# Performance work log

Measured on AMD Instinct MI355X. Metric: run time of the kernel, lower is better.

Reference implementation:

```python
import jax, jax.numpy as jnp
import numpy as np

B, T, C, H = 8, 1024, 1024, 16  # batch, seq, n_embd, n_head


def setup_inputs() -> dict:
    key = jax.random.key(0)
    ks = jax.random.split(key, 5)
    scale = 1.0 / np.sqrt(C)
    return {
        "x": jax.random.normal(ks[0], (B, T, C), dtype=jnp.float32),
        "Wqkv": jax.random.normal(ks[1], (C, 3 * C), dtype=jnp.float32) * scale,
        "bqkv": jax.random.normal(ks[2], (3 * C,), dtype=jnp.float32) * 0.02,
        "Wproj": jax.random.normal(ks[3], (C, C), dtype=jnp.float32) * scale,
        "bproj": jax.random.normal(ks[4], (C,), dtype=jnp.float32) * 0.02,
        "n_head": H,
    }


def reference(x, Wqkv, bqkv, Wproj, bproj, n_head):
    Bb, Tt, Cc = x.shape
    hd = Cc // n_head  # head dim
    qkv = x @ Wqkv + bqkv                      # [B,T,3C]
    q, k, v = jnp.split(qkv, 3, axis=-1)       # each [B,T,C]
    # [B,T,C] -> [B,H,T,hd]
    def to_heads(t):
        return t.reshape(Bb, Tt, n_head, hd).transpose(0, 2, 1, 3)
    q, k, v = to_heads(q), to_heads(k), to_heads(v)
    scores = jnp.einsum("bhqd,bhkd->bhqk", q, k) / jnp.sqrt(jnp.asarray(hd, q.dtype))
    causal = jnp.tril(jnp.ones((Tt, Tt), dtype=bool))
    scores = jnp.where(causal, scores, jnp.asarray(-jnp.inf, scores.dtype))
    attn = jax.nn.softmax(scores, axis=-1)
    y = jnp.einsum("bhqk,bhkd->bhqd", attn, v)  # [B,H,T,hd]
    y = y.transpose(0, 2, 1, 3).reshape(Bb, Tt, Cc)
    return y @ Wproj + bproj
```

## Files before the change

kernel.cpp:

```cpp
#include <hip/hip_runtime.h>
#include <hip/hip_bf16.h>
#include <math.h>
#include <type_traits>

#define Bz 8
#define Tz 1024
#define Cz 1024
#define Hz 16
#define HDz 64
#define Mz (Bz*Tz)
#define N1 (3*Cz)
#define QKN 2048

typedef __attribute__((ext_vector_type(8))) short short8;
typedef __attribute__((ext_vector_type(4))) short short4v;
typedef __attribute__((ext_vector_type(4))) float floatx4;

template<int V> using IC = std::integral_constant<int, V>;

__device__ __forceinline__ unsigned short f2bf(float f) {
    unsigned u = __float_as_uint(f);
    return (unsigned short)((u + 0x7FFFu + ((u >> 16) & 1u)) >> 16);
}

__device__ __forceinline__ unsigned pkbf(float a, float b) {
    __hip_bfloat162 h = __float22bfloat162_rn(make_float2(a, b));
    return *(unsigned*)&h;
}

__device__ __forceinline__ void gload16(const void* g, void* l) {
    __builtin_amdgcn_global_load_lds(
        (const __attribute__((address_space(1))) unsigned int*)g,
        (__attribute__((address_space(3))) unsigned int*)l, 16, 0, 0);
}

__global__ __launch_bounds__(256) void prep_kernel(
    const float* __restrict__ x, unsigned short* __restrict__ xb,
    const float* __restrict__ Wqkv, unsigned short* __restrict__ Wqkvt,
    const float* __restrict__ Wproj, unsigned short* __restrict__ Wprojt)
{
    __shared__ float tile[32][33];
    const int bid = blockIdx.x;
    const int tid = threadIdx.x;
    if (bid < 8192) {
        int i = bid * 256 + tid;
        float4 v = *(const float4*)&x[(size_t)i * 4];
        ushort4 o;
        o.x = f2bf(v.x); o.y = f2bf(v.y); o.z = f2bf(v.z); o.w = f2bf(v.w);
        *(ushort4*)&xb[(size_t)i * 4] = o;
        return;
    }
    const float* W; unsigned short* Wt; int K, N, n0, k0;
    if (bid < 11264) {
        int b = bid - 8192;  W = Wqkv;  Wt = Wqkvt;  K = Cz; N = N1;
        n0 = (b % 96) * 32;  k0 = (b / 96) * 32;
    } else {
        int b = bid - 11264; W = Wproj; Wt = Wprojt; K = Cz; N = Cz;
        n0 = (b % 32) * 32;  k0 = (b / 32) * 32;
    }
    const int tx = tid & 31, ty = tid >> 5;
#pragma unroll
    for (int i = 0; i < 4; ++i)
        tile[ty + i * 8][tx] = W[(size_t)(k0 + ty + i * 8) * N + n0 + tx];
    __syncthreads();
#pragma unroll
    for (int i = 0; i < 4; ++i)
        Wt[(size_t)(n0 + ty + i * 8) * K + k0 + tx] = f2bf(tile[tx][ty + i * 8]);
}

template<int NI, int MODE, int NXB>
__global__ __launch_bounds__(512) void gemm8p(
    const unsigned short* __restrict__ A,
    const unsigned short* __restrict__ Bt,
    const float* __restrict__ bias,
    void* __restrict__ Cout, unsigned short* __restrict__ VtG)
{
    constexpr int LDSB = 16384 + NI * 4096;
    constexpr int NT = 16;
    constexpr int NBLK = (Mz / 256) * NXB;
    constexpr int CHUNK = NBLK / 8;
    constexpr int NOUT = NXB * NI * 64;
    __shared__ unsigned short lds[2 * LDSB];

    const int tid = threadIdx.x;
    const int lane = tid & 63;
    const int w = tid >> 6;
    const int wm = w >> 2, wn = w & 3;
    const int quad = lane >> 4, m16 = lane & 15;
    const int sw7 = m16 & 7;

    int wg = blockIdx.x;
    wg = (wg & 7) * CHUNK + (wg >> 3);
    const int bx = wg % NXB, by = wg / NXB;
    const int row0 = by * 256, col0 = bx * (NI * 64);

    const int srow = tid >> 3;
    const int scol = ((tid & 7) ^ (srow & 7)) * 8;
    const unsigned short* sA[2][2];
    const unsigned short* sBu[NI];
#pragma unroll
    for (int h = 0; h < 2; ++h)
#pragma unroll
        for (int c = 0; c < 2; ++c)
            sA[h][c] = A + (size_t)(row0 + h * 128 + c * 64 + srow) * Cz + scol;
#pragma unroll
    for (int u = 0; u < NI; ++u)
        sBu[u] = Bt + (size_t)(col0 + u * 64 + srow) * Cz + scol;

    auto stage_tile = [&](int kt, int db) {
        unsigned short* base = &lds[db * LDSB];
#pragma unroll
        for (int u = 0; u < NI; ++u)
            gload16(sBu[u] + kt * 64, base + 16384 + u * 4096 + w * 512);
        gload16(sA[0][0] + kt * 64, base + w * 512);
        gload16(sA[0][1] + kt * 64, base + w * 512 + 4096);
        gload16(sA[1][0] + kt * 64, base + 8192 + w * 512);
        gload16(sA[1][1] + kt * 64, base + 8192 + w * 512 + 4096);
    };

    float bv[NI];
#pragma unroll
    for (int ni = 0; ni < NI; ++ni)
        bv[ni] = bias[col0 + wn * (NI * 16) + ni * 16 + m16];

    floatx4 acc[8][NI];
#pragma unroll
    for (int mi = 0; mi < 8; ++mi)
#pragma unroll
        for (int ni = 0; ni < NI; ++ni)
            acc[mi][ni] = (floatx4){0.f, 0.f, 0.f, 0.f};

    stage_tile(0, 0);
    stage_tile(1, 1);

    int b = 0;
#pragma unroll 1
    for (int kt = 0; kt < NT; ++kt, b ^= 1) {
        if (kt < NT - 1) {
            if constexpr (NI == 3) asm volatile("s_waitcnt vmcnt(7)" ::: "memory");
            else                   asm volatile("s_waitcnt vmcnt(6)" ::: "memory");
        } else {
            asm volatile("s_waitcnt vmcnt(0)" ::: "memory");
        }
        asm volatile("s_barrier" ::: "memory");

        const unsigned short* lA = &lds[b * LDSB];
        const unsigned short* lB = &lds[b * LDSB + 16384];

        auto loadA = [&](auto pc, short8 (&af)[2][2]) {
            constexpr int p = decltype(pc)::value;
            constexpr int hf = p >> 1;
#pragma unroll
            for (int j = 0; j < 2; ++j) {
                const int ra = ((p & 1) * 64 + j * 32 + wm * 16 + m16) * 64;
#pragma unroll
                for (int ks = 0; ks < 2; ++ks)
                    af[j][ks] = *(const short8*)&lA[hf * 8192 + ra + ((((ks << 2) | quad) ^ sw7) << 3)];
            }
        };

        short8 bfr[NI][2];
#pragma unroll
        for (int ni = 0; ni < NI; ++ni) {
            const int rb = (wn * (NI * 16) + ni * 16 + m16) * 64;
#pragma unroll
            for (int ks = 0; ks < 2; ++ks)
                bfr[ni][ks] = *(const short8*)&lB[rb + ((((ks << 2) | quad) ^ sw7) << 3)];
        }

        auto cluster = [&](auto pc, short8 (&af)[2][2]) {
            constexpr int p = decltype(pc)::value;
            __builtin_amdgcn_s_setprio(1);
#pragma unroll
            for (int ks = 0; ks < 2; ++ks)
#pragma unroll
                for (int j = 0; j < 2; ++j)
#pragma unroll
                    for (int ni = 0; ni < NI; ++ni)
                        acc[p * 2 + j][ni] = __builtin_amdgcn_mfma_f32_16x16x32_bf16(
                            af[j][ks], bfr[ni][ks], acc[p * 2 + j][ni], 0, 0, 0);
            __builtin_amdgcn_s_setprio(0);
        };

        short8 afA[2][2], afB[2][2];
        loadA(IC<0>{}, afA);
        __builtin_amdgcn_sched_barrier(0);
        loadA(IC<1>{}, afB);
        __builtin_amdgcn_sched_barrier(0);
        asm volatile("s_waitcnt lgkmcnt(4)" ::: "memory");
        __builtin_amdgcn_sched_barrier(0);
        cluster(IC<0>{}, afA);
        loadA(IC<2>{}, afA);
        __builtin_amdgcn_sched_barrier(0);
        asm volatile("s_waitcnt lgkmcnt(4)" ::: "memory");
        __builtin_amdgcn_sched_barrier(0);
        cluster(IC<1>{}, afB);
        loadA(IC<3>{}, afB);
        __builtin_amdgcn_sched_barrier(0);
        asm volatile("s_waitcnt lgkmcnt(4)" ::: "memory");
        __builtin_amdgcn_sched_barrier(0);
        cluster(IC<2>{}, afA);
        asm volatile("s_waitcnt lgkmcnt(0)" ::: "memory");
        __builtin_amdgcn_sched_barrier(0);
        if (kt + 2 < NT) {
            asm volatile("s_barrier" ::: "memory");
            stage_tile(kt + 2, b);
        }
        __builtin_amdgcn_sched_barrier(0);
        cluster(IC<3>{}, afB);
    }

    if constexpr (MODE == 0) {
#pragma unroll
        for (int ni = 0; ni < NI; ++ni) {
            const int c = col0 + wn * (NI * 16) + ni * 16 + m16;
#pragma unroll
            for (int mi = 0; mi < 8; ++mi)
#pragma unroll
                for (int reg = 0; reg < 4; ++reg) {
                    const int r = row0 + mi * 32 + wm * 16 + quad * 4 + reg;
                    ((float*)Cout)[(size_t)r * NOUT + c] = acc[mi][ni][reg] + bv[ni];
                }
        }
    } else {
#pragma unroll
        for (int ni = 0; ni < NI; ++ni) {
            const int c0 = col0 + wn * (NI * 16) + ni * 16;
            if (c0 < 2048) {
#pragma unroll
                for (int mi = 0; mi < 8; ++mi)
#pragma unroll
                    for (int reg = 0; reg < 4; ++reg) {
                        const int r = row0 + mi * 32 + wm * 16 + quad * 4 + reg;
                        ((unsigned short*)Cout)[(size_t)r * QKN + c0 + m16] =
                            f2bf(acc[mi][ni][reg] + bv[ni]);
                    }
            } else {
                const int cb = c0 - 2048;
                const int hsel = cb >> 6;
                const int dd = (cb & 63) + m16;
                const int bq = row0 >> 10;
                const int tb = row0 & 1023;
                unsigned short* drow = VtG
                    + (size_t)(bq * Hz + hsel) * (HDz * Tz)
                    + (size_t)dd * Tz + tb;
#pragma unroll
                for (int mi = 0; mi < 8; ++mi) {
                    const int t = mi * 32 + wm * 16 + quad * 4;
                    unsigned pk[2];
                    pk[0] = pkbf(acc[mi][ni][0] + bv[ni], acc[mi][ni][1] + bv[ni]);
                    pk[1] = pkbf(acc[mi][ni][2] + bv[ni], acc[mi][ni][3] + bv[ni]);
                    *(uint2*)&drow[t] = *(uint2*)pk;
                }
            }
        }
    }
}

__global__ __launch_bounds__(128) void attn_kernel(const unsigned short* __restrict__ qkb,
    const unsigned short* __restrict__ VtG, unsigned short* __restrict__ attb)
{
    __shared__ unsigned short Ks[2][64 * 64];
    __shared__ unsigned short Vs[2][64 * 64];

    const int bx = blockIdx.x;
    const int bh = blockIdx.y;
    const int b = bh >> 4, h = bh & 15;
    const int tid = threadIdx.x, lane = tid & 63, w = tid >> 6;
    const int quad = lane >> 4, m16 = lane & 15;
    const int qis[2] = {15 - bx, bx};

    const unsigned short* Kb = qkb + (size_t)(b * Tz) * QKN + Cz + h * HDz;
    const unsigned short* Vb = VtG + (size_t)bh * (HDz * Tz);

    const int l3 = lane >> 3, l7 = lane & 7;
    const int gsw = ((l7 ^ l3) << 3);
    const int sw = m16 & 7;
    const int p0 = (quad ^ sw) << 3;

    short8 onesf = (short8){0,0,0,0,0,0,0,0};
    if (m16 == 0) {
        const short one = (short)0x3F80;
        onesf = (short8){one,one,one,one,one,one,one,one};
    }

    int srow[4];
#pragma unroll
    for (int i = 0; i < 4; ++i) srow[i] = w * 32 + i * 8 + l3;

#pragma unroll
    for (int i = 0; i < 4; ++i) {
        gload16(Kb + (size_t)srow[i] * QKN + gsw, &Ks[0][(w * 4 + i) * 512]);
        gload16(Vb + (size_t)srow[i] * Tz + gsw, &Vs[0][(w * 4 + i) * 512]);
    }

    int buf = 0;
    for (int t = 0; t < 2; ++t) {
        const int qi = qis[t];

        short8 qf[2][2];
        int qrow[2];
#pragma unroll
        for (int mi = 0; mi < 2; ++mi) {
            qrow[mi] = qi * 64 + w * 32 + mi * 16 + m16;
            const size_t rq = (size_t)(b * Tz + qrow[mi]) * QKN + h * HDz;
            qf[mi][0] = *(const short8*)&qkb[rq + quad * 8];
            qf[mi][1] = *(const short8*)&qkb[rq + 32 + quad * 8];
        }

        floatx4 of[2][4];
#pragma unroll
        for (int mi = 0; mi < 2; ++mi)
#pragma unroll
            for (int dc = 0; dc < 4; ++dc) of[mi][dc] = (floatx4){0.f, 0.f, 0.f, 0.f};
        floatx4 lsum[2];
        lsum[0] = (floatx4){0.f, 0.f, 0.f, 0.f};
        lsum[1] = (floatx4){0.f, 0.f, 0.f, 0.f};

        auto tile_body = [&](auto diag_c) {
            constexpr bool DIAG = decltype(diag_c)::value;
            short8 pf[2][2];
#pragma unroll
            for (int m0 = 0; m0 < 4; ++m0) {
                if (DIAG && w == 0 && m0 >= 2) continue;
                const unsigned short* kr = &Ks[buf][(m0 * 16 + m16) * 64];
                short8 kf0 = *(const short8*)&kr[p0];
                short8 kf1 = *(const short8*)&kr[p0 ^ 32];
#pragma unroll
                for (int mi = 0; mi < 2; ++mi) {
                    floatx4 st = (floatx4){0.f, 0.f, 0.f, 0.f};
                    st = __builtin_amdgcn_mfma_f32_16x16x32_bf16(kf0, qf[mi][0], st, 0, 0, 0);
                    st = __builtin_amdgcn_mfma_f32_16x16x32_bf16(kf1, qf[mi][1], st, 0, 0, 0);
                    float p[4];
#pragma unroll
                    for (int reg = 0; reg < 4; ++reg) {
                        p[reg] = exp2f(st[reg] * 0.18033688f);
                        if (DIAG) {
                            int key = m0 * 16 + quad * 4 + reg;
                            int qr  = w * 32 + mi * 16 + m16;
                            p[reg] = (key <= qr) ? p[reg] : 0.f;
                        }
                    }
                    unsigned* pp = (unsigned*)&pf[mi][m0 >> 1];
                    pp[(m0 & 1) * 2 + 0] = pkbf(p[0], p[1]);
                    pp[(m0 & 1) * 2 + 1] = pkbf(p[2], p[3]);
                }
            }
#pragma unroll
            for (int kg = 0; kg < 2; ++kg) {
                if (DIAG && w == 0 && kg == 1) continue;
#pragma unroll
                for (int mi = 0; mi < 2; ++mi)
                    lsum[mi] = __builtin_amdgcn_mfma_f32_16x16x32_bf16(onesf, pf[mi][kg], lsum[mi], 0, 0, 0);
#pragma unroll
                for (int dc = 0; dc < 4; ++dc) {
                    const unsigned short* vrow = &Vs[buf][(dc * 16 + m16) * 64];
                    const int g0 = kg * 4 + (quad >> 1);
                    const int off = (quad & 1) * 4;
                    short4v v0 = *(const short4v*)&vrow[((g0 ^ sw) << 3) + off];
                    short4v v1 = *(const short4v*)&vrow[(((g0 + 2) ^ sw) << 3) + off];
                    short8 vf;
                    vf[0] = v0[0]; vf[1] = v0[1]; vf[2] = v0[2]; vf[3] = v0[3];
                    vf[4] = v1[0]; vf[5] = v1[1]; vf[6] = v1[2]; vf[7] = v1[3];
#pragma unroll
                    for (int mi = 0; mi < 2; ++mi)
                        of[mi][dc] = __builtin_amdgcn_mfma_f32_16x16x32_bf16(vf, pf[mi][kg], of[mi][dc], 0, 0, 0);
                }
            }
        };

        for (int ki = 0; ki <= qi; ++ki) {
            __syncthreads();
            const int nk = (ki < qi) ? (ki + 1) : (t == 0 ? 0 : -1);
            if (nk >= 0) {
                const size_t ko = (size_t)nk * 64;
#pragma unroll
                for (int i = 0; i < 4; ++i) {
                    gload16(Kb + (ko + srow[i]) * QKN + gsw, &Ks[buf ^ 1][(w * 4 + i) * 512]);
                    gload16(Vb + (size_t)srow[i] * Tz + ko + gsw, &Vs[buf ^ 1][(w * 4 + i) * 512]);
                }
            }
            if (ki == qi) tile_body(std::true_type{});
            else          tile_body(std::false_type{});
            buf ^= 1;
        }

#pragma unroll
        for (int mi = 0; mi < 2; ++mi) {
            const float l = __shfl(lsum[mi][0], m16);
            const float inv = 1.f / l;
            const size_t orow = (size_t)(b * Tz + qrow[mi]) * Cz + h * HDz;
#pragma unroll
            for (int dc = 0; dc < 4; ++dc) {
                ushort4 o;
                o.x = f2bf(of[mi][dc][0] * inv);
                o.y = f2bf(of[mi][dc][1] * inv);
                o.z = f2bf(of[mi][dc][2] * inv);
                o.w = f2bf(of[mi][dc][3] * inv);
                *(ushort4*)&attb[orow + dc * 16 + quad * 4] = o;
            }
        }
    }
}

extern "C" void kernel_launch(void* const* d_in, const int* in_sizes, int n_in,
                              void* d_out, int out_size, void* d_ws, size_t ws_size,
                              hipStream_t stream)
{
    const float* x     = (const float*)d_in[0];
    const float* Wqkv  = (const float*)d_in[1];
    const float* bqkv  = (const float*)d_in[2];
    const float* Wproj = (const float*)d_in[3];
    const float* bproj = (const float*)d_in[4];
    float* out = (float*)d_out;

    unsigned short* xb     = (unsigned short*)d_ws;
    unsigned short* Wqkvt  = xb + (size_t)Mz * Cz;
    unsigned short* Wprojt = Wqkvt + (size_t)N1 * Cz;
    unsigned short* qkb    = Wprojt + (size_t)Cz * Cz;
    unsigned short* VtG    = qkb + (size_t)Mz * QKN;
    unsigned short* attb   = xb;

    prep_kernel<<<12288, 256, 0, stream>>>(x, xb, Wqkv, Wqkvt, Wproj, Wprojt);

    gemm8p<3, 2, 16><<<512, 512, 0, stream>>>(xb, Wqkvt, bqkv, qkb, VtG);

    attn_kernel<<<dim3(8, Bz * Hz), 128, 0, stream>>>(qkb, VtG, attb);

    gemm8p<2, 0, 8><<<256, 512, 0, stream>>>(attb, Wprojt, bproj, out, nullptr);
}
```

Before: 236.0 us.

## Replace QKV GEMM with 128x192-tile kernel using split A/B staging

Adds a dedicated QKV projection kernel that uses 128x192 output tiles and 1024 workgroups, replacing the previous 256-row tile kernel launched with 512 workgroups. The new kernel staggers the A and B global loads across two half-iterations, raises MFMA priority during compute, and remaps block IDs for locality. The smaller LDS footprint and launch_bounds(512,4) aim to raise occupancy and smooth the memory pipeline, at the cost of less data reuse per tile. It also adds an explicit vmcnt(0) wait after the bias loads so they do not disturb the vmcnt-based pipeline accounting.

```diff
diff --git a/kernel.cpp b/kernel.cpp
--- a/kernel.cpp
+++ b/kernel.cpp
@@ -68,6 +68,158 @@
         Wt[(size_t)(n0 + ty + i * 8) * K + k0 + tx] = f2bf(tile[tx][ty + i * 8]);
 }
 
+__global__ __launch_bounds__(512, 4) void gemm128_qkv(
+    const unsigned short* __restrict__ A,
+    const unsigned short* __restrict__ Bt,
+    const float* __restrict__ bias,
+    unsigned short* __restrict__ Cqk, unsigned short* __restrict__ VtG)
+{
+    __shared__ unsigned short lds[2 * 20480];
+    constexpr int NT = 16;
+
+    const int tid = threadIdx.x;
+    const int lane = tid & 63;
+    const int w = tid >> 6;
+    const int wm = w >> 2, wn = w & 3;
+    const int quad = lane >> 4, m16 = lane & 15;
+    const int sw7 = m16 & 7;
+
+    int wg = blockIdx.x;
+    wg = (wg & 7) * 128 + (wg >> 3);
+    const int bx = wg & 15, by = wg >> 4;
+    const int row0 = by * 128, col0 = bx * 192;
+
+    const int srow = tid >> 3;
+    const int scol = ((tid & 7) ^ (srow & 7)) * 8;
+    const unsigned short* a0 = A  + (size_t)(row0 + srow) * Cz + scol;
+    const unsigned short* b0 = Bt + (size_t)(col0 + srow) * Cz + scol;
+
+    auto stageA = [&](int kt, int db) {
+        unsigned short* d = &lds[db * 20480 + w * 512];
+        gload16(a0 + kt * 64, d);
+        gload16(a0 + kt * 64 + 64 * Cz, d + 4096);
+    };
+    auto stageB = [&](int kt, int db) {
+        unsigned short* d = &lds[db * 20480 + 8192 + w * 512];
+        gload16(b0 + kt * 64, d);
+        gload16(b0 + kt * 64 + 64 * Cz, d + 4096);
+        gload16(b0 + kt * 64 + 128 * Cz, d + 8192);
+    };
+
+    float bv[3];
+#pragma unroll
+    for (int ni = 0; ni < 3; ++ni)
+        bv[ni] = bias[col0 + wn * 48 + ni * 16 + m16];
+    asm volatile("s_waitcnt vmcnt(0)" ::: "memory");
+
+    floatx4 acc[4][3];
+#pragma unroll
+    for (int mi = 0; mi < 4; ++mi)
+#pragma unroll
+        for (int ni = 0; ni < 3; ++ni)
+            acc[mi][ni] = (floatx4){0.f, 0.f, 0.f, 0.f};
+
+    stageA(0, 0); stageB(0, 0);
+    stageB(1, 1);
+    asm volatile("s_waitcnt vmcnt(3)" ::: "memory");
+    asm volatile("s_barrier" ::: "memory");
+
+    int b = 0;
+#pragma unroll 1
+    for (int kt = 0; kt < NT; ++kt, b ^= 1) {
+        const unsigned short* lA = &lds[b * 20480];
+        const unsigned short* lB = &lds[b * 20480 + 8192];
+
+        short8 bfr[3][2];
+#pragma unroll
+        for (int ni = 0; ni < 3; ++ni) {
+            const int rb = wn * 48 + ni * 16 + m16;
+#pragma unroll
+            for (int ks = 0; ks < 2; ++ks)
+                bfr[ni][ks] = *(const short8*)&lB[(rb >> 6) * 4096 + (rb & 63) * 64
+                                                  + ((((ks << 2) | quad) ^ sw7) << 3)];
+        }
+        short8 af[2][2];
+#pragma unroll
+        for (int jj = 0; jj < 2; ++jj)
+#pragma unroll
+            for (int ks = 0; ks < 2; ++ks)
+                af[jj][ks] = *(const short8*)&lA[wm * 4096 + (jj * 16 + m16) * 64
+                                                 + ((((ks << 2) | quad) ^ sw7) << 3)];
+        if (kt + 1 < NT) stageA(kt + 1, b ^ 1);
+        asm volatile("s_barrier" ::: "memory");
+        asm volatile("s_waitcnt lgkmcnt(0)" ::: "memory");
+        __builtin_amdgcn_sched_barrier(0);
+        __builtin_amdgcn_s_setprio(1);
+#pragma unroll
+        for (int ks = 0; ks < 2; ++ks)
+#pragma unroll
+            for (int jj = 0; jj < 2; ++jj)
+#pragma unroll
+                for (int ni = 0; ni < 3; ++ni)
+                    acc[jj][ni] = __builtin_amdgcn_mfma_f32_16x16x32_bf16(
+                        af[jj][ks], bfr[ni][ks], acc[jj][ni], 0, 0, 0);
+        __builtin_amdgcn_s_setprio(0);
+        asm volatile("s_barrier" ::: "memory");
+
+        short8 af2[2][2];
+#pragma unroll
+        for (int jj = 0; jj < 2; ++jj)
+#pragma unroll
+            for (int ks = 0; ks < 2; ++ks)
+                af2[jj][ks] = *(const short8*)&lA[wm * 4096 + ((2 + jj) * 16 + m16) * 64
+                                                  + ((((ks << 2) | quad) ^ sw7) << 3)];
+        if (kt + 2 < NT) stageB(kt + 2, b);
+        asm volatile("s_barrier" ::: "memory");
+        asm volatile("s_waitcnt lgkmcnt(0)" ::: "memory");
+        __builtin_amdgcn_sched_barrier(0);
+        __builtin_amdgcn_s_setprio(1);
+#pragma unroll
+        for (int ks = 0; ks < 2; ++ks)
+#pragma unroll
+            for (int jj = 0; jj < 2; ++jj)
+#pragma unroll
+                for (int ni = 0; ni < 3; ++ni)
+                    acc[2 + jj][ni] = __builtin_amdgcn_mfma_f32_16x16x32_bf16(
+                        af2[jj][ks], bfr[ni][ks], acc[2 + jj][ni], 0, 0, 0);
+        __builtin_amdgcn_s_setprio(0);
+        if (kt < NT - 2) { asm volatile("s_waitcnt vmcnt(3)" ::: "memory"); }
+        else             { asm volatile("s_waitcnt vmcnt(0)" ::: "memory"); }
+        asm volatile("s_barrier" ::: "memory");
+    }
+
+#pragma unroll
+    for (int ni = 0; ni < 3; ++ni) {
+        const int c0 = col0 + wn * 48 + ni * 16;
+        if (c0 < 2048) {
+#pragma unroll
+            for (int mi = 0; mi < 4; ++mi)
+#pragma unroll
+                for (int reg = 0; reg < 4; ++reg) {
+                    const int r = row0 + wm * 64 + mi * 16 + quad * 4 + reg;
+                    Cqk[(size_t)r * QKN + c0 + m16] = f2bf(acc[mi][ni][reg] + bv[ni]);
+                }
+        } else {
+            const int cb = c0 - 2048;
+            const int hsel = cb >> 6;
+            const int dd = (cb & 63) + m16;
+            const int bq = row0 >> 10;
+            const int tb = row0 & 1023;
+            unsigned short* drow = VtG
+                + (size_t)(bq * Hz + hsel) * (HDz * Tz)
+                + (size_t)dd * Tz + tb;
+#pragma unroll
+            for (int mi = 0; mi < 4; ++mi) {
+                const int t = wm * 64 + mi * 16 + quad * 4;
+                unsigned pk[2];
+                pk[0] = pkbf(acc[mi][ni][0] + bv[ni], acc[mi][ni][1] + bv[ni]);
+                pk[1] = pkbf(acc[mi][ni][2] + bv[ni], acc[mi][ni][3] + bv[ni]);
+                *(uint2*)&drow[t] = *(uint2*)pk;
+            }
+        }
+    }
+}
+
 template<int NI, int MODE, int NXB>
 __global__ __launch_bounds__(512) void gemm8p(
     const unsigned short* __restrict__ A,
@@ -122,6 +274,7 @@
 #pragma unroll
     for (int ni = 0; ni < NI; ++ni)
         bv[ni] = bias[col0 + wn * (NI * 16) + ni * 16 + m16];
+    asm volatile("s_waitcnt vmcnt(0)" ::: "memory");
 
     floatx4 acc[8][NI];
 #pragma unroll
@@ -423,7 +576,7 @@
 
     prep_kernel<<<12288, 256, 0, stream>>>(x, xb, Wqkv, Wqkvt, Wproj, Wprojt);
 
-    gemm8p<3, 2, 16><<<512, 512, 0, stream>>>(xb, Wqkvt, bqkv, qkb, VtG);
+    gemm128_qkv<<<1024, 512, 0, stream>>>(xb, Wqkvt, bqkv, qkb, VtG);
 
     attn_kernel<<<dim3(8, Bz * Hz), 128, 0, stream>>>(qkb, VtG, attb);
 
```

Result: no change. 237.1 us (+0.5%).
